# Kernel optimization log

Hardware: AMD Instinct MI355X
Metric: run time of the kernel (lower is better)

The kernel has to match this reference:

```python
import jax, jax.numpy as jnp
import numpy as np

BATCH = 1024
D = 256          # input_size == embed_size (forced by elementwise multiply)
NUM_REL = 42     # num_classes + 2
FEAT = 30


def setup_inputs() -> dict:
    key = jax.random.key(0)
    k_x, k_q, k_f, k_r = jax.random.split(key, 4)
    x = jax.random.normal(k_x, (BATCH, D), dtype=jnp.float32)
    x_mask = jnp.ones((BATCH,), dtype=bool)  # unused by the module body
    q = jax.random.randint(k_q, (BATCH, BATCH), 0, NUM_REL, dtype=jnp.int64)
    f = jax.random.normal(k_f, (BATCH, FEAT), dtype=jnp.float32)  # unused by the module body
    # relation embedding table, init std=0.001, row 0 zeroed (padding relation)
    R_emb = jax.random.normal(k_r, (NUM_REL, D), dtype=jnp.float32) * 0.001
    R_emb = R_emb.at[0].set(0.0)
    return {"x": x, "x_mask": x_mask, "q": q, "f": f, "R_emb": R_emb}


def reference(x, x_mask, q, f, R_emb):
    # r[i,j,d] = R_emb[q[i,j], d]   (the big O(B^2*D) gather)
    r = R_emb[q]  # [B, B, D]
    # attn[i,j] = sum_d r[i,j,d] * x[j,d] * x[i,d]
    attn = jnp.einsum('ijd,jd,id->ij', r, x, x)  # [B, B]
    weights = jax.nn.softmax(attn, axis=-1)
    outputs = weights @ x  # [B, D]
    return outputs
```

## Files before the change

### kernel.cpp

```cpp
#include <hip/hip_runtime.h>
#include <hip/hip_bf16.h>

#define BB 1024
#define DD 256
#define NREL 42
#define AST 264

typedef __attribute__((ext_vector_type(8))) short short8_t;
typedef __attribute__((ext_vector_type(4))) short short4_t;
typedef __attribute__((ext_vector_type(4))) float f32x4;
typedef __attribute__((ext_vector_type(4))) int   i32x4;
typedef __attribute__((ext_vector_type(4))) unsigned int u32x4;

__device__ __forceinline__ unsigned short bf16_of(float f) {
    unsigned u = __float_as_uint(f);
    return (unsigned short)((u + 0x7FFFu + ((u >> 16) & 1u)) >> 16);
}

__device__ __forceinline__ float blo(unsigned u) { return __uint_as_float(u << 16); }
__device__ __forceinline__ float bhi(unsigned u) { return __uint_as_float(u & 0xFFFF0000u); }

__device__ __forceinline__ void dot8bf2(u32x4 aa, u32x4 ab, u32x4 xv,
                                        float& ra, float& rb) {
    #pragma unroll
    for (int e = 0; e < 4; ++e) {
        const float xl = blo(xv[e]);
        const float xh = bhi(xv[e]);
        ra = fmaf(blo(aa[e]), xl, ra);
        ra = fmaf(bhi(aa[e]), xh, ra);
        rb = fmaf(blo(ab[e]), xl, rb);
        rb = fmaf(bhi(ab[e]), xh, rb);
    }
}

__global__ __launch_bounds__(256) void cvt_kernel(const float* __restrict__ x,
                                                  unsigned short* __restrict__ xh8,
                                                  unsigned short* __restrict__ xbfT) {
    __shared__ float t32[64][68];
    const int bj = blockIdx.x * 64;
    const int bd = blockIdx.y * 64;
    const int tid = threadIdx.x;
    const int tr = tid >> 4;
    const int tc = tid & 15;

    #pragma unroll
    for (int rr = 0; rr < 4; ++rr) {
        const int jl = rr * 16 + tr;
        const f32x4 v = *reinterpret_cast<const f32x4*>(&x[(bj + jl) * DD + bd + tc * 4]);
        *reinterpret_cast<f32x4*>(&t32[jl][tc * 4]) = v;
    }
    __syncthreads();

    #pragma unroll
    for (int rr = 0; rr < 4; ++rr) {
        const int dl = rr * 16 + tr;
        short4_t h;
        #pragma unroll
        for (int e = 0; e < 4; ++e) h[e] = (short)bf16_of(t32[tc * 4 + e][dl]);
        *reinterpret_cast<short4_t*>(&xbfT[(bd + dl) * BB + bj + tc * 4]) = h;
    }

    #pragma unroll
    for (int c = 0; c < 2; ++c) {
        const int idx = c * 256 + tid;
        const int jl  = idx & 63;
        const int d8l = idx >> 6;
        short8_t hv;
        #pragma unroll
        for (int e = 0; e < 8; ++e) hv[e] = (short)bf16_of(t32[jl][d8l * 8 + e]);
        *reinterpret_cast<short8_t*>(
            &xh8[(size_t)((bd >> 3) + d8l) * (BB * 8) + (bj + jl) * 8]) = hv;
    }
}

__global__ __launch_bounds__(256) void attn_kernel(const float* __restrict__ x,
                                                   const int* __restrict__ q,
                                                   const float* __restrict__ R,
                                                   const unsigned short* __restrict__ xh8,
                                                   unsigned short* __restrict__ P) {
    __shared__ __align__(16) unsigned short Ah[2][NREL * AST];
    __shared__ float s_attn[2][BB];
    __shared__ unsigned short s_qs[2][BB];

    const int tid  = threadIdx.x;
    const int w    = tid >> 6;
    const int lane = tid & 63;
    const int i0   = blockIdx.x * 2;

    {
        const int r  = tid >> 7;
        const int c8 = (tid & 127) * 8;
        const int qi = i0 + r;
        const i32x4 qa = *reinterpret_cast<const i32x4*>(&q[qi * BB + c8]);
        const i32x4 qb = *reinterpret_cast<const i32x4*>(&q[qi * BB + c8 + 4]);
        short4_t sa, sb;
        sa[0] = (short)qa[0]; sa[1] = (short)qa[1]; sa[2] = (short)qa[2]; sa[3] = (short)qa[3];
        sb[0] = (short)qb[0]; sb[1] = (short)qb[1]; sb[2] = (short)qb[2]; sb[3] = (short)qb[3];
        *reinterpret_cast<short4_t*>(&s_qs[r][c8])     = sa;
        *reinterpret_cast<short4_t*>(&s_qs[r][c8 + 4]) = sb;
    }

    #pragma unroll
    for (int i2 = 0; i2 < 2; ++i2) {
        const int i = i0 + i2;
        for (int c = tid; c < NREL * 32; c += 256) {
            const int k  = c >> 5;
            const int d0 = (c & 31) * 8;
            const f32x4 r0 = *reinterpret_cast<const f32x4*>(&R[k * DD + d0]);
            const f32x4 r1 = *reinterpret_cast<const f32x4*>(&R[k * DD + d0 + 4]);
            const f32x4 x0 = *reinterpret_cast<const f32x4*>(&x[i * DD + d0]);
            const f32x4 x1 = *reinterpret_cast<const f32x4*>(&x[i * DD + d0 + 4]);
            short8_t hv;
            #pragma unroll
            for (int e = 0; e < 4; ++e) {
                hv[e]     = (short)bf16_of(r0[e] * x0[e]);
                hv[e + 4] = (short)bf16_of(r1[e] * x1[e]);
            }
            *reinterpret_cast<short8_t*>(&Ah[i2][k * AST + d0]) = hv;
        }
    }

    __syncthreads();

    const int j0 = w * 256 + lane;
    const unsigned short* a00 = &Ah[0][(int)s_qs[0][j0]       * AST];
    const unsigned short* a01 = &Ah[0][(int)s_qs[0][j0 + 64]  * AST];
    const unsigned short* a02 = &Ah[0][(int)s_qs[0][j0 + 128] * AST];
    const unsigned short* a03 = &Ah[0][(int)s_qs[0][j0 + 192] * AST];
    const unsigned short* a10 = &Ah[1][(int)s_qs[1][j0]       * AST];
    const unsigned short* a11 = &Ah[1][(int)s_qs[1][j0 + 64]  * AST];
    const unsigned short* a12 = &Ah[1][(int)s_qs[1][j0 + 128] * AST];
    const unsigned short* a13 = &Ah[1][(int)s_qs[1][j0 + 192] * AST];
    const unsigned short* xp = xh8 + (size_t)j0 * 8;

    float c00 = 0.f, c01 = 0.f, c02 = 0.f, c03 = 0.f;
    float c10 = 0.f, c11 = 0.f, c12 = 0.f, c13 = 0.f;

    #pragma unroll 2
    for (int d8 = 0; d8 < 32; ++d8) {
        const unsigned short* xb = xp + (size_t)d8 * (BB * 8);
        const u32x4 xv0 = *reinterpret_cast<const u32x4*>(xb);
        const u32x4 xv1 = *reinterpret_cast<const u32x4*>(xb + 64 * 8);
        const u32x4 xv2 = *reinterpret_cast<const u32x4*>(xb + 128 * 8);
        const u32x4 xv3 = *reinterpret_cast<const u32x4*>(xb + 192 * 8);

        const int ao = d8 * 8;
        const u32x4 av00 = *reinterpret_cast<const u32x4*>(a00 + ao);
        const u32x4 av01 = *reinterpret_cast<const u32x4*>(a01 + ao);
        const u32x4 av02 = *reinterpret_cast<const u32x4*>(a02 + ao);
        const u32x4 av03 = *reinterpret_cast<const u32x4*>(a03 + ao);
        const u32x4 av10 = *reinterpret_cast<const u32x4*>(a10 + ao);
        const u32x4 av11 = *reinterpret_cast<const u32x4*>(a11 + ao);
        const u32x4 av12 = *reinterpret_cast<const u32x4*>(a12 + ao);
        const u32x4 av13 = *reinterpret_cast<const u32x4*>(a13 + ao);

        dot8bf2(av00, av10, xv0, c00, c10);
        dot8bf2(av01, av11, xv1, c01, c11);
        dot8bf2(av02, av12, xv2, c02, c12);
        dot8bf2(av03, av13, xv3, c03, c13);
    }

    s_attn[0][j0]       = c00;  s_attn[1][j0]       = c10;
    s_attn[0][j0 + 64]  = c01;  s_attn[1][j0 + 64]  = c11;
    s_attn[0][j0 + 128] = c02;  s_attn[1][j0 + 128] = c12;
    s_attn[0][j0 + 192] = c03;  s_attn[1][j0 + 192] = c13;

    __syncthreads();

    const int p2 = w & 1;
    const int jh = w >> 1;
    const int i  = i0 + p2;

    f32x4 v4[4];
    #pragma unroll
    for (int kk = 0; kk < 4; ++kk)
        v4[kk] = *reinterpret_cast<const f32x4*>(&s_attn[p2][kk * 256 + lane * 4]);

    float m = -1e30f;
    #pragma unroll
    for (int kk = 0; kk < 4; ++kk)
        m = fmaxf(m, fmaxf(fmaxf(v4[kk][0], v4[kk][1]), fmaxf(v4[kk][2], v4[kk][3])));
    #pragma unroll
    for (int off = 1; off < 64; off <<= 1) m = fmaxf(m, __shfl_xor(m, off));

    float e[16];
    float ssum = 0.f;
    #pragma unroll
    for (int kk = 0; kk < 4; ++kk)
        #pragma unroll
        for (int ee = 0; ee < 4; ++ee) {
            const float t2 = __expf(v4[kk][ee] - m);
            e[kk * 4 + ee] = t2;
            ssum += t2;
        }
    #pragma unroll
    for (int off = 1; off < 64; off <<= 1) ssum += __shfl_xor(ssum, off);
    const float inv = 1.0f / ssum;

    #pragma unroll
    for (int kk2 = 0; kk2 < 2; ++kk2) {
        const int kk = jh * 2 + kk2;
        short4_t pv;
        #pragma unroll
        for (int ee = 0; ee < 4; ++ee) pv[ee] = (short)bf16_of(e[kk * 4 + ee] * inv);
        *reinterpret_cast<short4_t*>(&P[i * BB + kk * 256 + lane * 4]) = pv;
    }
}

__global__ __launch_bounds__(256) void out_partial(const unsigned short* __restrict__ P,
                                                   const unsigned short* __restrict__ xbfT,
                                                   float* __restrict__ part) {
    const int tid = threadIdx.x;
    const int wave = tid >> 6, lane = tid & 63;
    const int lcol = lane & 15;
    const int lk8  = (lane >> 4) * 8;
    const int i0 = blockIdx.y * 64 + wave * 16;
    const int d0 = blockIdx.x * 64;
    const int k0 = blockIdx.z * 256;

    f32x4 acc[4];
    #pragma unroll
    for (int nt = 0; nt < 4; ++nt) acc[nt] = (f32x4)0.0f;

    #pragma unroll
    for (int ks = 0; ks < 8; ++ks) {
        const short8_t a = *reinterpret_cast<const short8_t*>(
            &P[(i0 + lcol) * BB + k0 + ks * 32 + lk8]);
        #pragma unroll
        for (int nt = 0; nt < 4; ++nt) {
            const short8_t b = *reinterpret_cast<const short8_t*>(
                &xbfT[(d0 + nt * 16 + lcol) * BB + k0 + ks * 32 + lk8]);
            acc[nt] = __builtin_amdgcn_mfma_f32_16x16x32_bf16(a, b, acc[nt], 0, 0, 0);
        }
    }

    const int rbase = (lane >> 4) * 4;
    float* pz = part + (size_t)blockIdx.z * BB * DD;
    #pragma unroll
    for (int r = 0; r < 4; ++r)
        #pragma unroll
        for (int nt = 0; nt < 4; ++nt)
            pz[(i0 + rbase + r) * DD + d0 + nt * 16 + lcol] = acc[nt][r];
}

__global__ __launch_bounds__(256) void out_reduce(const float* __restrict__ part,
                                                  float* __restrict__ out) {
    const int idx = blockIdx.x * DD + threadIdx.x;
    out[idx] = (part[idx] + part[BB * DD + idx]) +
               (part[2 * BB * DD + idx] + part[3 * BB * DD + idx]);
}

extern "C" void kernel_launch(void* const* d_in, const int* in_sizes, int n_in,
                              void* d_out, int out_size, void* d_ws, size_t ws_size,
                              hipStream_t stream) {
    (void)in_sizes; (void)n_in; (void)out_size; (void)ws_size;
    const float* x = (const float*)d_in[0];
    const int* q = (const int*)d_in[2];
    const float* R = (const float*)d_in[4];
    float* out = (float*)d_out;

    char* ws = (char*)d_ws;
    unsigned short* xh8  = (unsigned short*)(ws);
    unsigned short* xbfT = (unsigned short*)(ws + (512u << 10));
    unsigned short* P    = (unsigned short*)(ws + (1024u << 10));
    float*          part = (float*)(ws + (3072u << 10));

    cvt_kernel<<<dim3(16, 4), 256, 0, stream>>>(x, xh8, xbfT);
    attn_kernel<<<dim3(512), 256, 0, stream>>>(x, q, R, xh8, P);
    out_partial<<<dim3(4, 16, 4), 256, 0, stream>>>(P, xbfT, part);
    out_reduce<<<dim3(BB), 256, 0, stream>>>(part, out);
}
```

Before: 43.79 us.

## Process four query rows per attention block to reuse x loads

The attention kernel now handles four rows i per block with 512 threads instead of two rows with 256 threads. Each thread covers two j columns for all four rows, so each bf16 x vector read from global memory feeds four dot products instead of two. This halves the global/L2 traffic for x in the score phase. In exchange, LDS use per block roughly doubles and there are half as many blocks, which may lower occupancy or leave compute units idle.

Measured after the change: 42.75 us. 1.02x faster.

```diff
diff --git a/kernel.cpp b/kernel.cpp
--- a/kernel.cpp
+++ b/kernel.cpp
@@ -20,16 +20,17 @@
 __device__ __forceinline__ float blo(unsigned u) { return __uint_as_float(u << 16); }
 __device__ __forceinline__ float bhi(unsigned u) { return __uint_as_float(u & 0xFFFF0000u); }
 
-__device__ __forceinline__ void dot8bf2(u32x4 aa, u32x4 ab, u32x4 xv,
-                                        float& ra, float& rb) {
+__device__ __forceinline__ void dot8bf4(u32x4 a0, u32x4 a1, u32x4 a2, u32x4 a3,
+                                        u32x4 xv,
+                                        float& r0, float& r1, float& r2, float& r3) {
     #pragma unroll
     for (int e = 0; e < 4; ++e) {
         const float xl = blo(xv[e]);
         const float xh = bhi(xv[e]);
-        ra = fmaf(blo(aa[e]), xl, ra);
-        ra = fmaf(bhi(aa[e]), xh, ra);
-        rb = fmaf(blo(ab[e]), xl, rb);
-        rb = fmaf(bhi(ab[e]), xh, rb);
+        r0 = fmaf(blo(a0[e]), xl, r0);  r0 = fmaf(bhi(a0[e]), xh, r0);
+        r1 = fmaf(blo(a1[e]), xl, r1);  r1 = fmaf(bhi(a1[e]), xh, r1);
+        r2 = fmaf(blo(a2[e]), xl, r2);  r2 = fmaf(bhi(a2[e]), xh, r2);
+        r3 = fmaf(blo(a3[e]), xl, r3);  r3 = fmaf(bhi(a3[e]), xh, r3);
     }
 }
 
@@ -73,19 +74,19 @@
     }
 }
 
-__global__ __launch_bounds__(256) void attn_kernel(const float* __restrict__ x,
+__global__ __launch_bounds__(512) void attn_kernel(const float* __restrict__ x,
                                                    const int* __restrict__ q,
                                                    const float* __restrict__ R,
                                                    const unsigned short* __restrict__ xh8,
                                                    unsigned short* __restrict__ P) {
-    __shared__ __align__(16) unsigned short Ah[2][NREL * AST];
-    __shared__ float s_attn[2][BB];
-    __shared__ unsigned short s_qs[2][BB];
+    __shared__ __align__(16) unsigned short Ah[4][NREL * AST];
+    __shared__ float s_attn[4][BB];
+    __shared__ unsigned short s_qs[4][BB];
 
     const int tid  = threadIdx.x;
     const int w    = tid >> 6;
     const int lane = tid & 63;
-    const int i0   = blockIdx.x * 2;
+    const int i0   = blockIdx.x * 4;
 
     {
         const int r  = tid >> 7;
@@ -101,9 +102,9 @@
     }
 
     #pragma unroll
-    for (int i2 = 0; i2 < 2; ++i2) {
+    for (int i2 = 0; i2 < 4; ++i2) {
         const int i = i0 + i2;
-        for (int c = tid; c < NREL * 32; c += 256) {
+        for (int c = tid; c < NREL * 32; c += 512) {
             const int k  = c >> 5;
             const int d0 = (c & 31) * 8;
             const f32x4 r0 = *reinterpret_cast<const f32x4*>(&R[k * DD + d0]);
@@ -122,53 +123,49 @@
 
     __syncthreads();
 
-    const int j0 = w * 256 + lane;
-    const unsigned short* a00 = &Ah[0][(int)s_qs[0][j0]       * AST];
-    const unsigned short* a01 = &Ah[0][(int)s_qs[0][j0 + 64]  * AST];
-    const unsigned short* a02 = &Ah[0][(int)s_qs[0][j0 + 128] * AST];
-    const unsigned short* a03 = &Ah[0][(int)s_qs[0][j0 + 192] * AST];
-    const unsigned short* a10 = &Ah[1][(int)s_qs[1][j0]       * AST];
-    const unsigned short* a11 = &Ah[1][(int)s_qs[1][j0 + 64]  * AST];
-    const unsigned short* a12 = &Ah[1][(int)s_qs[1][j0 + 128] * AST];
-    const unsigned short* a13 = &Ah[1][(int)s_qs[1][j0 + 192] * AST];
-    const unsigned short* xp = xh8 + (size_t)j0 * 8;
-
-    float c00 = 0.f, c01 = 0.f, c02 = 0.f, c03 = 0.f;
-    float c10 = 0.f, c11 = 0.f, c12 = 0.f, c13 = 0.f;
+    const int j0 = tid;
+    const int j1 = tid + 512;
+    const unsigned short* a00 = &Ah[0][(int)s_qs[0][j0] * AST];
+    const unsigned short* a10 = &Ah[1][(int)s_qs[1][j0] * AST];
+    const unsigned short* a20 = &Ah[2][(int)s_qs[2][j0] * AST];
+    const unsigned short* a30 = &Ah[3][(int)s_qs[3][j0] * AST];
+    const unsigned short* a01 = &Ah[0][(int)s_qs[0][j1] * AST];
+    const unsigned short* a11 = &Ah[1][(int)s_qs[1][j1] * AST];
+    const unsigned short* a21 = &Ah[2][(int)s_qs[2][j1] * AST];
+    const unsigned short* a31 = &Ah[3][(int)s_qs[3][j1] * AST];
+    const unsigned short* xp0 = xh8 + (size_t)j0 * 8;
+    const unsigned short* xp1 = xh8 + (size_t)j1 * 8;
+
+    float c00 = 0.f, c10 = 0.f, c20 = 0.f, c30 = 0.f;
+    float c01 = 0.f, c11 = 0.f, c21 = 0.f, c31 = 0.f;
 
     #pragma unroll 2
     for (int d8 = 0; d8 < 32; ++d8) {
-        const unsigned short* xb = xp + (size_t)d8 * (BB * 8);
-        const u32x4 xv0 = *reinterpret_cast<const u32x4*>(xb);
-        const u32x4 xv1 = *reinterpret_cast<const u32x4*>(xb + 64 * 8);
-        const u32x4 xv2 = *reinterpret_cast<const u32x4*>(xb + 128 * 8);
-        const u32x4 xv3 = *reinterpret_cast<const u32x4*>(xb + 192 * 8);
+        const size_t xo = (size_t)d8 * (BB * 8);
+        const u32x4 xv0 = *reinterpret_cast<const u32x4*>(xp0 + xo);
+        const u32x4 xv1 = *reinterpret_cast<const u32x4*>(xp1 + xo);
 
         const int ao = d8 * 8;
         const u32x4 av00 = *reinterpret_cast<const u32x4*>(a00 + ao);
+        const u32x4 av10 = *reinterpret_cast<const u32x4*>(a10 + ao);
+        const u32x4 av20 = *reinterpret_cast<const u32x4*>(a20 + ao);
+        const u32x4 av30 = *reinterpret_cast<const u32x4*>(a30 + ao);
         const u32x4 av01 = *reinterpret_cast<const u32x4*>(a01 + ao);
-        const u32x4 av02 = *reinterpret_cast<const u32x4*>(a02 + ao);
-        const u32x4 av03 = *reinterpret_cast<const u32x4*>(a03 + ao);
-        const u32x4 av10 = *reinterpret_cast<const u32x4*>(a10 + ao);
         const u32x4 av11 = *reinterpret_cast<const u32x4*>(a11 + ao);
-        const u32x4 av12 = *reinterpret_cast<const u32x4*>(a12 + ao);
-        const u32x4 av13 = *reinterpret_cast<const u32x4*>(a13 + ao);
-
-        dot8bf2(av00, av10, xv0, c00, c10);
-        dot8bf2(av01, av11, xv1, c01, c11);
-        dot8bf2(av02, av12, xv2, c02, c12);
-        dot8bf2(av03, av13, xv3, c03, c13);
-    }
-
-    s_attn[0][j0]       = c00;  s_attn[1][j0]       = c10;
-    s_attn[0][j0 + 64]  = c01;  s_attn[1][j0 + 64]  = c11;
-    s_attn[0][j0 + 128] = c02;  s_attn[1][j0 + 128] = c12;
-    s_attn[0][j0 + 192] = c03;  s_attn[1][j0 + 192] = c13;
+        const u32x4 av21 = *reinterpret_cast<const u32x4*>(a21 + ao);
+        const u32x4 av31 = *reinterpret_cast<const u32x4*>(a31 + ao);
+
+        dot8bf4(av00, av10, av20, av30, xv0, c00, c10, c20, c30);
+        dot8bf4(av01, av11, av21, av31, xv1, c01, c11, c21, c31);
+    }
+
+    s_attn[0][j0] = c00;  s_attn[1][j0] = c10;  s_attn[2][j0] = c20;  s_attn[3][j0] = c30;
+    s_attn[0][j1] = c01;  s_attn[1][j1] = c11;  s_attn[2][j1] = c21;  s_attn[3][j1] = c31;
 
     __syncthreads();
 
-    const int p2 = w & 1;
-    const int jh = w >> 1;
+    const int p2 = w >> 1;
+    const int jh = w & 1;
     const int i  = i0 + p2;
 
     f32x4 v4[4];
@@ -266,7 +263,7 @@
     float*          part = (float*)(ws + (3072u << 10));
 
     cvt_kernel<<<dim3(16, 4), 256, 0, stream>>>(x, xh8, xbfT);
-    attn_kernel<<<dim3(512), 256, 0, stream>>>(x, q, R, xh8, P);
+    attn_kernel<<<dim3(256), 512, 0, stream>>>(x, q, R, xh8, P);
     out_partial<<<dim3(4, 16, 4), 256, 0, stream>>>(P, xbfT, part);
     out_reduce<<<dim3(BB), 256, 0, stream>>>(part, out);
 }
```
